# Kernel optimization log

Hardware: AMD Instinct MI355X
Metric: run time of the kernel (lower is better)

Reference implementation:

```python
import jax, jax.numpy as jnp
import numpy as np

B, S, F, DV, H, DH, L = 32, 600, 9, 1024, 16, 64, 2


def setup_inputs() -> dict:
    key = jax.random.key(0)
    ks = jax.random.split(key, 24)
    w = lambda k, shape, s=0.05: jax.random.normal(k, shape, dtype=jnp.float32) * s
    return {
        "x": w(ks[0], (B, S, F), 1.0),
        "enc_in_W": w(ks[1], (F, DV)), "enc_in_b": w(ks[2], (DV,)),
        "Wq": w(ks[3], (L, H, DV, DH)), "bq": w(ks[4], (L, H, DH)),
        "Wk": w(ks[5], (L, H, DV, DH)), "bk": w(ks[6], (L, H, DH)),
        "Wv": w(ks[7], (L, H, DV, DH)), "bv": w(ks[8], (L, H, DH)),
        "Wo": w(ks[9], (L, DV, DV)), "bo": w(ks[10], (L, DV)),
        "W1": w(ks[11], (L, DV, DV)), "b1": w(ks[12], (L, DV)),
        "W2": w(ks[13], (L, DV, DV)), "b2": w(ks[14], (L, DV)),
        "ln1_w": jnp.ones((L, DV)), "ln1_b": jnp.zeros((L, DV)),
        "ln2_w": jnp.ones((L, DV)), "ln2_b": jnp.zeros((L, DV)),
        "out_W": w(ks[15], (DV, F)), "out_b": w(ks[16], (F,)),
    }


def _layernorm(v, g, b):
    mu = v.mean(-1, keepdims=True)
    var = v.var(-1, keepdims=True)  # biased, matches torch LayerNorm
    return (v - mu) / jnp.sqrt(var + 1e-5) * g + b


def reference(x, enc_in_W, enc_in_b, Wq, bq, Wk, bk, Wv, bv, Wo, bo,
              W1, b1, W2, b2, ln1_w, ln1_b, ln2_w, ln2_b, out_W, out_b):
    # enc_input_fc; pe skipped (code checks pe_mode == 'stardard', never true)
    h = x @ enc_in_W + enc_in_b  # [B,S,DV]
    scale = 1.0 / jnp.sqrt(jnp.float32(DH))
    for l in range(L):
        q = jnp.einsum('bsd,hdk->bhsk', h, Wq[l]) + bq[l][None, :, None, :]
        k = jnp.einsum('bsd,hdk->bhsk', h, Wk[l]) + bk[l][None, :, None, :]
        v = jnp.einsum('bsd,hdk->bhsk', h, Wv[l]) + bv[l][None, :, None, :]
        attn = jax.nn.softmax(jnp.einsum('bhsk,bhtk->bhst', q, k) * scale, axis=-1)
        ctx = jnp.einsum('bhst,bhtk->bhsk', attn, v)  # [B,H,S,DH]
        # torch: stack(heads, dim=-1) -> [B,S,DH,H], then flatten(start_dim=2)
        a = ctx.transpose(0, 2, 3, 1).reshape(B, S, DH * H)
        attn_out = a @ Wo[l] + bo[l]
        x1 = _layernorm(h + attn_out, ln1_w[l], ln1_b[l])
        ff = jax.nn.elu(x1 @ W2[l] + b2[l]) @ W1[l] + b1[l]  # fc1(elu(fc2(x1)))
        h = _layernorm(x1 + ff, ln2_w[l], ln2_b[l])
    out = h @ out_W + out_b  # [B,S,F]; in_seq_len == out_seq_len -> no out_seq_fc
    return out
```

## Files before the change

kernel.cpp:

```cpp
#include <hip/hip_runtime.h>

typedef unsigned short u16;
typedef unsigned int u32;
typedef __attribute__((ext_vector_type(8))) short shortx8;
typedef __attribute__((ext_vector_type(4))) float floatx4;
typedef __attribute__((ext_vector_type(4))) u32 uintx4;
typedef __attribute__((ext_vector_type(2))) u32 uintx2;

#define AS1 __attribute__((address_space(1)))
#define AS3 __attribute__((address_space(3)))

__device__ __forceinline__ float bf2f(u16 u) {
  return __builtin_bit_cast(float, ((u32)u) << 16);
}
__device__ __forceinline__ u16 f2bf(float f) {
  u32 i = __builtin_bit_cast(u32, f);
  u32 r = (i + 0x7fffu + ((i >> 16) & 1u)) >> 16;
  return (u16)r;
}
__device__ __forceinline__ u16 f2bf_rtz(float f) {
  return (u16)(__builtin_bit_cast(u32, f) >> 16);
}

__launch_bounds__(256)
__global__ void pack_all(const float* __restrict__ Wq, const float* __restrict__ Wk,
                         const float* __restrict__ Wv, const float* __restrict__ Wo,
                         const float* __restrict__ W1, const float* __restrict__ W2,
                         const float* __restrict__ bq, const float* __restrict__ bk,
                         const float* __restrict__ bv,
                         u16* __restrict__ Bqkv, u16* __restrict__ Bwo,
                         u16* __restrict__ Bw1, u16* __restrict__ Bw2,
                         float* __restrict__ bias) {
  __shared__ u16 T[64 * 72];
  const int blk = blockIdx.x;
  const int t = threadIdx.x;

  if (blk < 1536) {
    const int which = blk >> 9, r = blk & 511;
    const int kt = r & 15, y = r >> 4;
    const float* W = (which == 0) ? Wq : (which == 1) ? Wk : Wv;
    u16* dst = Bqkv + (size_t)which * 1048576;
    const int l = y >> 4, h = y & 15;
    const int rr = t >> 2, cq = (t & 3) * 16;
    const float* src = W + ((size_t)y * 1024 + kt * 64 + rr) * 64 + cq;
#pragma unroll
    for (int e4 = 0; e4 < 4; ++e4) {
      float4 f = *(const float4*)(src + e4 * 4);
      T[(cq + e4 * 4 + 0) * 72 + rr] = f2bf(f.x);
      T[(cq + e4 * 4 + 1) * 72 + rr] = f2bf(f.y);
      T[(cq + e4 * 4 + 2) * 72 + rr] = f2bf(f.z);
      T[(cq + e4 * 4 + 3) * 72 + rr] = f2bf(f.w);
    }
    __syncthreads();
    const int dd = t >> 2, kq = (t & 3) * 16;
    u16* drow = dst + (size_t)l * 3145728 + ((size_t)h * 64 + dd) * 1024 + kt * 64 + kq;
    *(uintx4*)(drow) = *(const uintx4*)&T[dd * 72 + kq];
    *(uintx4*)(drow + 8) = *(const uintx4*)&T[dd * 72 + kq + 8];
  } else if (blk < 2048) {
    const int r = blk - 1536;
    const int l = r >> 8, rx = r & 255;
    const int rt = rx >> 4, nt = rx & 15;
    const int rr = t >> 2, cq = (t & 3) * 16;
    const float* src = Wo + (size_t)l * 1048576 + (size_t)(rt * 64 + rr) * 1024 + nt * 64 + cq;
#pragma unroll
    for (int e4 = 0; e4 < 4; ++e4) {
      float4 f = *(const float4*)(src + e4 * 4);
      T[(cq + e4 * 4 + 0) * 72 + rr] = f2bf(f.x);
      T[(cq + e4 * 4 + 1) * 72 + rr] = f2bf(f.y);
      T[(cq + e4 * 4 + 2) * 72 + rr] = f2bf(f.z);
      T[(cq + e4 * 4 + 3) * 72 + rr] = f2bf(f.w);
    }
    __syncthreads();
    const int hh = t & 15;
#pragma unroll
    for (int pass = 0; pass < 4; ++pass) {
      const int nl = pass * 16 + (t >> 4);
      uintx2 pk;
      u16 v0 = T[nl * 72 + 0 * 16 + hh], v1 = T[nl * 72 + 1 * 16 + hh];
      u16 v2 = T[nl * 72 + 2 * 16 + hh], v3 = T[nl * 72 + 3 * 16 + hh];
      pk[0] = (u32)v0 | ((u32)v1 << 16);
      pk[1] = (u32)v2 | ((u32)v3 << 16);
      *(uintx2*)&Bwo[(size_t)l * 1048576 + (size_t)(nt * 64 + nl) * 1024 + hh * 64 + rt * 4] = pk;
    }
  } else if (blk < 3072) {
    const int job = (blk - 2048) >> 9;
    const int r = (blk - 2048) & 511;
    const float* W = job == 0 ? W1 : W2;
    u16* dst = job == 0 ? Bw1 : Bw2;
    const int l = r >> 8, rx = r & 255;
    const int ct = rx & 15, rt = rx >> 4;
    const int rr = t >> 2, cq = (t & 3) * 16;
    const float* src = W + (size_t)l * 1048576 + (size_t)(rt * 64 + rr) * 1024 + ct * 64 + cq;
#pragma unroll
    for (int e4 = 0; e4 < 4; ++e4) {
      float4 f = *(const float4*)(src + e4 * 4);
      T[(cq + e4 * 4 + 0) * 72 + rr] = f2bf(f.x);
      T[(cq + e4 * 4 + 1) * 72 + rr] = f2bf(f.y);
      T[(cq + e4 * 4 + 2) * 72 + rr] = f2bf(f.z);
      T[(cq + e4 * 4 + 3) * 72 + rr] = f2bf(f.w);
    }
    __syncthreads();
    const int cc = t >> 2, rq = (t & 3) * 16;
    u16* drow = dst + (size_t)l * 1048576 + (size_t)(ct * 64 + cc) * 1024 + rt * 64 + rq;
    *(uintx4*)(drow) = *(const uintx4*)&T[cc * 72 + rq];
    *(uintx4*)(drow + 8) = *(const uintx4*)&T[cc * 72 + rq + 8];
  } else {
    const int i = (blk - 3072) * 256 + t;
    const int l = i / 3072, n = i % 3072;
    const int which = n >> 10, nn = n & 1023;
    const float* s = (which == 0) ? bq : (which == 1) ? bk : bv;
    bias[i] = s[l * 1024 + nn];
  }
}

__launch_bounds__(256)
__global__ void enc_kernel(const float* __restrict__ x, const float* __restrict__ W,
                           const float* __restrict__ bias, u16* __restrict__ h) {
  const size_t i = (size_t)blockIdx.x * 256 + threadIdx.x;
  const int m = (int)(i >> 7), nq = (int)((i & 127) << 3);
  const float* xr = x + (size_t)m * 9;
  float xv[9];
#pragma unroll
  for (int f = 0; f < 9; ++f) xv[f] = xr[f];
  u16 ov[8];
#pragma unroll
  for (int e = 0; e < 8; ++e) {
    float acc = bias[nq + e];
#pragma unroll
    for (int f = 0; f < 9; ++f) acc += xv[f] * W[f * 1024 + nq + e];
    ov[e] = f2bf(acc);
  }
  *(uintx4*)&h[(size_t)m * 1024 + nq] = *(const uintx4*)ov;
}

template <int EPI>
__launch_bounds__(512)
__global__ void gemm_bt_wide(const u16* __restrict__ A, int lda,
                             const u16* __restrict__ Bt,
                             const float* __restrict__ bias,
                             const u16* __restrict__ R, int ldr,
                             u16* __restrict__ C, int ldc) {
  constexpr int K = 1024;
  __shared__ u16 As[128 * 64];
  __shared__ u16 Bs[256 * 64];
  const int tid = threadIdx.x;
  const int lane = tid & 63;
  const int w = tid >> 6;
  const int wr = w >> 2, wc = w & 3;
  const int m0 = blockIdx.y * 128, n0 = blockIdx.x * 256;

  floatx4 acc[4][4];
#pragma unroll
  for (int i = 0; i < 4; ++i)
#pragma unroll
    for (int j = 0; j < 4; ++j) acc[i][j] = (floatx4){0.f, 0.f, 0.f, 0.f};

  const u16* Ab = A + (size_t)m0 * lda;
  const u16* Bb = Bt + (size_t)n0 * K;

  for (int k0 = 0; k0 < K; k0 += 64) {
#pragma unroll
    for (int p = 0; p < 2; ++p) {
      const int o = p * 8192 + tid * 16;
      const int row = o >> 7;
      const int ke = (o & 127) >> 1;
      __builtin_amdgcn_global_load_lds((const AS1 void*)(Ab + (size_t)row * lda + (k0 + ke)),
                                       (AS3 void*)((char*)As + o), 16, 0, 0);
    }
#pragma unroll
    for (int p = 0; p < 4; ++p) {
      const int o = p * 8192 + tid * 16;
      const int row = o >> 7;
      const int ke = (o & 127) >> 1;
      __builtin_amdgcn_global_load_lds((const AS1 void*)(Bb + (size_t)row * K + (k0 + ke)),
                                       (AS3 void*)((char*)Bs + o), 16, 0, 0);
    }
    __syncthreads();
#pragma unroll
    for (int ks = 0; ks < 2; ++ks) {
      shortx8 af[4], bfr[4];
#pragma unroll
      for (int i = 0; i < 4; ++i) {
        const int ar = wr * 64 + i * 16 + (lane & 15);
        af[i] = *(const shortx8*)&As[ar * 64 + ks * 32 + (lane >> 4) * 8];
        const int br = wc * 64 + i * 16 + (lane & 15);
        bfr[i] = *(const shortx8*)&Bs[br * 64 + ks * 32 + (lane >> 4) * 8];
      }
#pragma unroll
      for (int i = 0; i < 4; ++i)
#pragma unroll
        for (int j = 0; j < 4; ++j)
          acc[i][j] = __builtin_amdgcn_mfma_f32_16x16x32_bf16(af[i], bfr[j], acc[i][j], 0, 0, 0);
    }
    __syncthreads();
  }

  const int lr = (lane >> 4) * 4, lc = lane & 15;
#pragma unroll
  for (int i = 0; i < 4; ++i) {
#pragma unroll
    for (int j = 0; j < 4; ++j) {
      const int col = n0 + wc * 64 + j * 16 + lc;
      const float bv = bias[col];
      const bool qcol = (EPI == 3) && (col < 1024);
#pragma unroll
      for (int r = 0; r < 4; ++r) {
        const int row = m0 + wr * 64 + i * 16 + lr + r;
        float v = acc[i][j][r] + bv;
        if (EPI == 1) v += bf2f(R[(size_t)row * ldr + col]);
        if (EPI == 2) v = v > 0.f ? v : expm1f(v);
        if (EPI == 3 && qcol) v *= 0.125f;
        C[(size_t)row * ldc + col] = f2bf(v);
      }
    }
  }
}

__launch_bounds__(256)
__global__ void attn_mfma(const u16* __restrict__ qkv, u16* __restrict__ aout) {
  const int qt = blockIdx.x, bh = blockIdx.y;
  const int b = bh >> 4, h = bh & 15;
  const int tid = threadIdx.x, lane = tid & 63, w = tid >> 6;
  const int g = lane >> 4, lq = lane & 15;

  __shared__ u16 K_ld[128 * 72];
  __shared__ u16 Vt[64 * 136];
  __shared__ u16 P_ld[4][16 * 136];

  const size_t bbase = (size_t)b * 600 * 3072;
  const int q0 = qt * 128 + w * 32;

  shortx8 aq[2][2];
#pragma unroll
  for (int sub = 0; sub < 2; ++sub) {
    const int s = q0 + sub * 16 + lq;
    if (s < 600) {
      const u16* qp = qkv + bbase + (size_t)s * 3072 + h * 64 + g * 8;
      aq[sub][0] = *(const shortx8*)qp;
      aq[sub][1] = *(const shortx8*)(qp + 32);
    } else {
      aq[sub][0] = (shortx8){0, 0, 0, 0, 0, 0, 0, 0};
      aq[sub][1] = (shortx8){0, 0, 0, 0, 0, 0, 0, 0};
    }
  }

  floatx4 Oa[2][4];
  float m[2][4], l[2][4];
#pragma unroll
  for (int sub = 0; sub < 2; ++sub) {
#pragma unroll
    for (int db = 0; db < 4; ++db) Oa[sub][db] = (floatx4){0.f, 0.f, 0.f, 0.f};
#pragma unroll
    for (int r = 0; r < 4; ++r) { m[sub][r] = -1e30f; l[sub][r] = 0.f; }
  }

  for (int ch = 0; ch < 5; ++ch) {
    const int t0 = ch * 128;
    __syncthreads();
    {
      const int tloc = tid >> 1, dhalf = (tid & 1) * 32;
      const int tp = t0 + lane * 2;
      const int dq = w * 16;
      if (ch < 4) {
        const u16* kp = qkv + bbase + (size_t)(t0 + tloc) * 3072 + 1024 + h * 64 + dhalf;
#pragma unroll
        for (int c = 0; c < 4; ++c)
          *(uintx4*)&K_ld[tloc * 72 + dhalf + c * 8] = *(const uintx4*)(kp + c * 8);
        const u16* vp0 = qkv + bbase + (size_t)tp * 3072 + 2048 + h * 64 + dq;
        const u16* vp1 = vp0 + 3072;
        shortx8 r0a = *(const shortx8*)vp0;
        shortx8 r0b = *(const shortx8*)(vp0 + 8);
        shortx8 r1a = *(const shortx8*)vp1;
        shortx8 r1b = *(const shortx8*)(vp1 + 8);
#pragma unroll
        for (int e = 0; e < 8; ++e) {
          *(u32*)&Vt[(dq + e) * 136 + lane * 2] =
              (u32)(u16)r0a[e] | ((u32)(u16)r1a[e] << 16);
          *(u32*)&Vt[(dq + 8 + e) * 136 + lane * 2] =
              (u32)(u16)r0b[e] | ((u32)(u16)r1b[e] << 16);
        }
      } else {
        const int tg = t0 + tloc;
        if (tg < 600) {
          const u16* kp = qkv + bbase + (size_t)tg * 3072 + 1024 + h * 64 + dhalf;
#pragma unroll
          for (int c = 0; c < 4; ++c)
            *(uintx4*)&K_ld[tloc * 72 + dhalf + c * 8] = *(const uintx4*)(kp + c * 8);
        } else {
          const uintx4 z4 = (uintx4){0, 0, 0, 0};
#pragma unroll
          for (int c = 0; c < 4; ++c)
            *(uintx4*)&K_ld[tloc * 72 + dhalf + c * 8] = z4;
        }
        shortx8 r0a, r0b, r1a, r1b;
        if (tp < 600) {
          const u16* vp = qkv + bbase + (size_t)tp * 3072 + 2048 + h * 64 + dq;
          r0a = *(const shortx8*)vp;
          r0b = *(const shortx8*)(vp + 8);
        } else {
          r0a = (shortx8){0, 0, 0, 0, 0, 0, 0, 0};
          r0b = r0a;
        }
        if (tp + 1 < 600) {
          const u16* vp = qkv + bbase + (size_t)(tp + 1) * 3072 + 2048 + h * 64 + dq;
          r1a = *(const shortx8*)vp;
          r1b = *(const shortx8*)(vp + 8);
        } else {
          r1a = (shortx8){0, 0, 0, 0, 0, 0, 0, 0};
          r1b = r1a;
        }
#pragma unroll
        for (int e = 0; e < 8; ++e) {
          *(u32*)&Vt[(dq + e) * 136 + lane * 2] =
              (u32)(u16)r0a[e] | ((u32)(u16)r1a[e] << 16);
          *(u32*)&Vt[(dq + 8 + e) * 136 + lane * 2] =
              (u32)(u16)r0b[e] | ((u32)(u16)r1b[e] << 16);
        }
      }
    }
    __syncthreads();

#pragma unroll
    for (int sub = 0; sub < 2; ++sub) {
      floatx4 S[8];
      __builtin_amdgcn_s_setprio(1);
#pragma unroll
      for (int jb = 0; jb < 8; ++jb) {
        S[jb] = (floatx4){0.f, 0.f, 0.f, 0.f};
#pragma unroll
        for (int ks = 0; ks < 2; ++ks) {
          shortx8 bk = *(const shortx8*)&K_ld[(jb * 16 + lq) * 72 + ks * 32 + g * 8];
          S[jb] = __builtin_amdgcn_mfma_f32_16x16x32_bf16(aq[sub][ks], bk, S[jb], 0, 0, 0);
        }
      }
      __builtin_amdgcn_s_setprio(0);
      if (ch == 4) {
#pragma unroll
        for (int jb = 0; jb < 8; ++jb) {
          const bool ok = (t0 + jb * 16 + lq) < 600;
#pragma unroll
          for (int r = 0; r < 4; ++r) S[jb][r] = ok ? S[jb][r] : -1e30f;
        }
      }

      float vmax[4];
      bool need = false;
#pragma unroll
      for (int r = 0; r < 4; ++r) {
        const float v01 = fmaxf(S[0][r], S[1][r]);
        const float v23 = fmaxf(S[2][r], S[3][r]);
        const float v45 = fmaxf(S[4][r], S[5][r]);
        const float v67 = fmaxf(S[6][r], S[7][r]);
        float v = fmaxf(fmaxf(v01, v23), fmaxf(v45, v67));
        v = fmaxf(v, __shfl_xor(v, 1));
        v = fmaxf(v, __shfl_xor(v, 2));
        v = fmaxf(v, __shfl_xor(v, 4));
        v = fmaxf(v, __shfl_xor(v, 8));
        vmax[r] = v;
        need |= (v > m[sub][r] + 8.0f);
      }
      if (__any(need ? 1 : 0)) {
#pragma unroll
        for (int r = 0; r < 4; ++r) {
          const float mn = fmaxf(m[sub][r], vmax[r]);
          const float sc = __expf(m[sub][r] - mn);
          m[sub][r] = mn;
          l[sub][r] *= sc;
#pragma unroll
          for (int db = 0; db < 4; ++db) Oa[sub][db][r] *= sc;
        }
      }

      float sums[4] = {0.f, 0.f, 0.f, 0.f};
#pragma unroll
      for (int jb = 0; jb < 8; ++jb)
#pragma unroll
        for (int r = 0; r < 4; ++r) {
          const float p = __expf(S[jb][r] - m[sub][r]);
          sums[r] += p;
          P_ld[w][(g * 4 + r) * 136 + jb * 16 + lq] = f2bf_rtz(p);
        }
#pragma unroll
      for (int r = 0; r < 4; ++r) {
        float v = sums[r];
        v += __shfl_xor(v, 1);
        v += __shfl_xor(v, 2);
        v += __shfl_xor(v, 4);
        v += __shfl_xor(v, 8);
        l[sub][r] += v;
      }

      __builtin_amdgcn_s_setprio(1);
#pragma unroll
      for (int ks = 0; ks < 4; ++ks) {
        shortx8 ap = *(const shortx8*)&P_ld[w][lq * 136 + ks * 32 + g * 8];
#pragma unroll
        for (int db = 0; db < 4; ++db) {
          shortx8 bv = *(const shortx8*)&Vt[(db * 16 + lq) * 136 + ks * 32 + g * 8];
          Oa[sub][db] = __builtin_amdgcn_mfma_f32_16x16x32_bf16(ap, bv, Oa[sub][db], 0, 0, 0);
        }
      }
      __builtin_amdgcn_s_setprio(0);
    }
  }

#pragma unroll
  for (int sub = 0; sub < 2; ++sub) {
#pragma unroll
    for (int r = 0; r < 4; ++r) {
      const int sg = q0 + sub * 16 + g * 4 + r;
      if (sg < 600) {
        const float inv = 1.f / l[sub][r];
        u16* orow = aout + ((size_t)(b * 600 + sg)) * 1024 + h * 64;
#pragma unroll
        for (int db = 0; db < 4; ++db)
          orow[db * 16 + lq] = f2bf(Oa[sub][db][r] * inv);
      }
    }
  }
}

__launch_bounds__(256)
__global__ void ln_kernel(const u16* __restrict__ y, int ldy,
                          const float* __restrict__ g, const float* __restrict__ be,
                          u16* __restrict__ o, int ldo) {
  const int row = blockIdx.x, tid = threadIdx.x;
  const int lane = tid & 63, wv = tid >> 6;
  const u16* yr = y + (size_t)row * ldy;
  const int c = tid * 4;
  const uintx2 yv = *(const uintx2*)&yr[c];
  float v0 = bf2f((u16)(yv[0] & 0xffffu)), v1 = bf2f((u16)(yv[0] >> 16));
  float v2 = bf2f((u16)(yv[1] & 0xffffu)), v3 = bf2f((u16)(yv[1] >> 16));
  float s = v0 + v1 + v2 + v3;
  float q = v0 * v0 + v1 * v1 + v2 * v2 + v3 * v3;
#pragma unroll
  for (int m = 32; m; m >>= 1) {
    s += __shfl_xor(s, m);
    q += __shfl_xor(q, m);
  }
  __shared__ float red[2][4];
  if (lane == 0) {
    red[0][wv] = s;
    red[1][wv] = q;
  }
  __syncthreads();
  s = red[0][0] + red[0][1] + red[0][2] + red[0][3];
  q = red[1][0] + red[1][1] + red[1][2] + red[1][3];
  const float mu = s * (1.f / 1024.f);
  const float var = q * (1.f / 1024.f) - mu * mu;
  const float rstd = rsqrtf(var + 1e-5f);
  const float4 gv = *(const float4*)&g[c];
  const float4 bev = *(const float4*)&be[c];
  const float o0 = (v0 - mu) * rstd * gv.x + bev.x;
  const float o1 = (v1 - mu) * rstd * gv.y + bev.y;
  const float o2 = (v2 - mu) * rstd * gv.z + bev.z;
  const float o3 = (v3 - mu) * rstd * gv.w + bev.w;
  uintx2 ov;
  ov[0] = (u32)f2bf(o0) | ((u32)f2bf(o1) << 16);
  ov[1] = (u32)f2bf(o2) | ((u32)f2bf(o3) << 16);
  *(uintx2*)&o[(size_t)row * ldo + c] = ov;
}

__launch_bounds__(256)
__global__ void out_kernel(const u16* __restrict__ h, const float* __restrict__ W,
                           const float* __restrict__ bias, float* __restrict__ out) {
  const int m = blockIdx.x * 4 + (threadIdx.x >> 6);
  const int lane = threadIdx.x & 63;
  float acc[9];
#pragma unroll
  for (int f = 0; f < 9; ++f) acc[f] = 0.f;
  const u16* hr = h + (size_t)m * 1024;
#pragma unroll 4
  for (int j = 0; j < 16; ++j) {
    const int k = lane + j * 64;
    const float hv = bf2f(hr[k]);
    const float* wr = W + (size_t)k * 9;
#pragma unroll
    for (int f = 0; f < 9; ++f) acc[f] += hv * wr[f];
  }
#pragma unroll
  for (int f = 0; f < 9; ++f)
#pragma unroll
    for (int mm = 32; mm; mm >>= 1) acc[f] += __shfl_xor(acc[f], mm);
  if (lane < 9) out[(size_t)m * 9 + lane] = acc[lane] + bias[lane];
}

extern "C" void kernel_launch(void* const* d_in, const int* in_sizes, int n_in,
                              void* d_out, int out_size, void* d_ws, size_t ws_size,
                              hipStream_t stream) {
  (void)in_sizes; (void)n_in; (void)out_size; (void)ws_size;
  const float* x     = (const float*)d_in[0];
  const float* encW  = (const float*)d_in[1];
  const float* encB  = (const float*)d_in[2];
  const float* Wq    = (const float*)d_in[3];
  const float* bq    = (const float*)d_in[4];
  const float* Wk    = (const float*)d_in[5];
  const float* bk    = (const float*)d_in[6];
  const float* Wv    = (const float*)d_in[7];
  const float* bv    = (const float*)d_in[8];
  const float* Wo    = (const float*)d_in[9];
  const float* bo    = (const float*)d_in[10];
  const float* W1    = (const float*)d_in[11];
  const float* b1    = (const float*)d_in[12];
  const float* W2    = (const float*)d_in[13];
  const float* b2    = (const float*)d_in[14];
  const float* ln1w  = (const float*)d_in[15];
  const float* ln1b  = (const float*)d_in[16];
  const float* ln2w  = (const float*)d_in[17];
  const float* ln2b  = (const float*)d_in[18];
  const float* outW  = (const float*)d_in[19];
  const float* outB  = (const float*)d_in[20];
  float* out = (float*)d_out;

  char* ws = (char*)d_ws;
  size_t off = 0;
  auto alloc = [&](size_t bytes) -> void* {
    void* p = ws + off;
    off += (bytes + 255) & ~(size_t)255;
    return p;
  };
  u16* h    = (u16*)alloc(19660800ull * 2);
  u16* qkv  = (u16*)alloc(58982400ull * 2);
  u16* abuf = (u16*)alloc(19660800ull * 2);
  u16* Bqkv = (u16*)alloc(6291456ull * 2);
  u16* Bwo  = (u16*)alloc(2097152ull * 2);
  u16* Bw1  = (u16*)alloc(2097152ull * 2);
  u16* Bw2  = (u16*)alloc(2097152ull * 2);
  float* bqkv = (float*)alloc(6144ull * 4);
  u16* ybuf = qkv;
  u16* x1   = qkv + 1024;
  u16* mid  = qkv + 2048;
  u16* y2   = abuf;

  pack_all<<<3096, 256, 0, stream>>>(Wq, Wk, Wv, Wo, W1, W2, bq, bk, bv,
                                     Bqkv, Bwo, Bw1, Bw2, bqkv);
  enc_kernel<<<9600, 256, 0, stream>>>(x, encW, encB, h);

  for (int l = 0; l < 2; ++l) {
    gemm_bt_wide<3><<<dim3(12, 150), 512, 0, stream>>>(
        h, 1024, Bqkv + (size_t)l * 3145728, bqkv + l * 3072, nullptr, 0, qkv, 3072);
    attn_mfma<<<dim3(5, 512), 256, 0, stream>>>(qkv, abuf);
    gemm_bt_wide<1><<<dim3(4, 150), 512, 0, stream>>>(
        abuf, 1024, Bwo + (size_t)l * 1048576, bo + l * 1024, h, 1024, ybuf, 3072);
    ln_kernel<<<19200, 256, 0, stream>>>(ybuf, 3072, ln1w + l * 1024, ln1b + l * 1024, x1, 3072);
    gemm_bt_wide<2><<<dim3(4, 150), 512, 0, stream>>>(
        x1, 3072, Bw2 + (size_t)l * 1048576, b2 + l * 1024, nullptr, 0, mid, 3072);
    gemm_bt_wide<1><<<dim3(4, 150), 512, 0, stream>>>(
        mid, 3072, Bw1 + (size_t)l * 1048576, b1 + l * 1024, x1, 3072, y2, 1024);
    ln_kernel<<<19200, 256, 0, stream>>>(y2, 1024, ln2w + l * 1024, ln2b + l * 1024, h, 1024);
  }
  out_kernel<<<4800, 256, 0, stream>>>(h, outW, outB, out);
}
```

Measured before the change: 1.241 ms.

## Use 256x256 QKV GEMM tile and prefetch K/V chunks in attention

Adds a dedicated QKV projection kernel with a 256x256 output tile and 1024 threads per block. This halves the number of times each weight tile is reloaded across row blocks and improves operand reuse per LDS load. The attention kernel now loads the next K/V chunk into registers while the current chunk is being processed, hiding global latency behind MFMA work. The cost is higher register pressure and fewer resident blocks per CU, and the 75x12 grid gives fewer blocks to balance across CUs.

```diff
diff --git a/kernel.cpp b/kernel.cpp
--- a/kernel.cpp
+++ b/kernel.cpp
@@ -131,6 +131,85 @@
     ov[e] = f2bf(acc);
   }
   *(uintx4*)&h[(size_t)m * 1024 + nq] = *(const uintx4*)ov;
+}
+
+__launch_bounds__(1024)
+__global__ void gemm_qkv_256(const u16* __restrict__ A,
+                             const u16* __restrict__ Bt,
+                             const float* __restrict__ bias,
+                             u16* __restrict__ C) {
+  constexpr int K = 1024;
+  __shared__ u16 As[256 * 64];
+  __shared__ u16 Bs[256 * 64];
+  const int tid = threadIdx.x;
+  const int lane = tid & 63;
+  const int w = tid >> 6;
+  const int wr = w >> 2, wc = w & 3;
+  const int m0 = blockIdx.y * 256, n0 = blockIdx.x * 256;
+
+  floatx4 acc[4][4];
+#pragma unroll
+  for (int i = 0; i < 4; ++i)
+#pragma unroll
+    for (int j = 0; j < 4; ++j) acc[i][j] = (floatx4){0.f, 0.f, 0.f, 0.f};
+
+  const u16* Ab = A + (size_t)m0 * K;
+  const u16* Bb = Bt + (size_t)n0 * K;
+
+  for (int k0 = 0; k0 < K; k0 += 64) {
+#pragma unroll
+    for (int p = 0; p < 2; ++p) {
+      const int o = p * 16384 + tid * 16;
+      const int row = o >> 7;
+      const int ke = (o & 127) >> 1;
+      __builtin_amdgcn_global_load_lds((const AS1 void*)(Ab + (size_t)row * K + (k0 + ke)),
+                                       (AS3 void*)((char*)As + o), 16, 0, 0);
+    }
+#pragma unroll
+    for (int p = 0; p < 2; ++p) {
+      const int o = p * 16384 + tid * 16;
+      const int row = o >> 7;
+      const int ke = (o & 127) >> 1;
+      __builtin_amdgcn_global_load_lds((const AS1 void*)(Bb + (size_t)row * K + (k0 + ke)),
+                                       (AS3 void*)((char*)Bs + o), 16, 0, 0);
+    }
+    __syncthreads();
+#pragma unroll
+    for (int ks = 0; ks < 2; ++ks) {
+      shortx8 af[4], bfr[4];
+#pragma unroll
+      for (int i = 0; i < 4; ++i) {
+        const int ar = wr * 64 + i * 16 + (lane & 15);
+        af[i] = *(const shortx8*)&As[ar * 64 + ks * 32 + (lane >> 4) * 8];
+        const int br = wc * 64 + i * 16 + (lane & 15);
+        bfr[i] = *(const shortx8*)&Bs[br * 64 + ks * 32 + (lane >> 4) * 8];
+      }
+#pragma unroll
+      for (int i = 0; i < 4; ++i)
+#pragma unroll
+        for (int j = 0; j < 4; ++j)
+          acc[i][j] = __builtin_amdgcn_mfma_f32_16x16x32_bf16(af[i], bfr[j], acc[i][j], 0, 0, 0);
+    }
+    __syncthreads();
+  }
+
+  const int lr = (lane >> 4) * 4, lc = lane & 15;
+#pragma unroll
+  for (int i = 0; i < 4; ++i) {
+#pragma unroll
+    for (int j = 0; j < 4; ++j) {
+      const int col = n0 + wc * 64 + j * 16 + lc;
+      const float bv = bias[col];
+      const bool qcol = col < 1024;
+#pragma unroll
+      for (int r = 0; r < 4; ++r) {
+        const int row = m0 + wr * 64 + i * 16 + lr + r;
+        float v = acc[i][j][r] + bv;
+        if (qcol) v *= 0.125f;
+        C[(size_t)row * 3072 + col] = f2bf(v);
+      }
+    }
+  }
 }
 
 template <int EPI>
@@ -202,14 +281,12 @@
     for (int j = 0; j < 4; ++j) {
       const int col = n0 + wc * 64 + j * 16 + lc;
       const float bv = bias[col];
-      const bool qcol = (EPI == 3) && (col < 1024);
 #pragma unroll
       for (int r = 0; r < 4; ++r) {
         const int row = m0 + wr * 64 + i * 16 + lr + r;
         float v = acc[i][j][r] + bv;
         if (EPI == 1) v += bf2f(R[(size_t)row * ldr + col]);
         if (EPI == 2) v = v > 0.f ? v : expm1f(v);
-        if (EPI == 3 && qcol) v *= 0.125f;
         C[(size_t)row * ldc + col] = f2bf(v);
       }
     }
@@ -229,6 +306,8 @@
 
   const size_t bbase = (size_t)b * 600 * 3072;
   const int q0 = qt * 128 + w * 32;
+  const int tloc = tid >> 1, dhalf = (tid & 1) * 32;
+  const int dq = w * 16;
 
   shortx8 aq[2][2];
 #pragma unroll
@@ -254,70 +333,68 @@
     for (int r = 0; r < 4; ++r) { m[sub][r] = -1e30f; l[sub][r] = 0.f; }
   }
 
+  uintx4 kreg[4];
+  shortx8 vra, vrb, vrc, vrd;
+
+  auto LOADC = [&](int ch) {
+    const int t0 = ch * 128;
+    if (ch < 4) {
+      const u16* kp = qkv + bbase + (size_t)(t0 + tloc) * 3072 + 1024 + h * 64 + dhalf;
+#pragma unroll
+      for (int c = 0; c < 4; ++c) kreg[c] = *(const uintx4*)(kp + c * 8);
+      const u16* vp0 = qkv + bbase + (size_t)(t0 + lane * 2) * 3072 + 2048 + h * 64 + dq;
+      vra = *(const shortx8*)vp0;
+      vrb = *(const shortx8*)(vp0 + 8);
+      vrc = *(const shortx8*)(vp0 + 3072);
+      vrd = *(const shortx8*)(vp0 + 3072 + 8);
+    } else {
+      const int tg = t0 + tloc;
+      if (tg < 600) {
+        const u16* kp = qkv + bbase + (size_t)tg * 3072 + 1024 + h * 64 + dhalf;
+#pragma unroll
+        for (int c = 0; c < 4; ++c) kreg[c] = *(const uintx4*)(kp + c * 8);
+      } else {
+#pragma unroll
+        for (int c = 0; c < 4; ++c) kreg[c] = (uintx4){0, 0, 0, 0};
+      }
+      const int tp = t0 + lane * 2;
+      if (tp < 600) {
+        const u16* vp = qkv + bbase + (size_t)tp * 3072 + 2048 + h * 64 + dq;
+        vra = *(const shortx8*)vp;
+        vrb = *(const shortx8*)(vp + 8);
+      } else {
+        vra = (shortx8){0, 0, 0, 0, 0, 0, 0, 0};
+        vrb = vra;
+      }
+      if (tp + 1 < 600) {
+        const u16* vp = qkv + bbase + (size_t)(tp + 1) * 3072 + 2048 + h * 64 + dq;
+        vrc = *(const shortx8*)vp;
+        vrd = *(const shortx8*)(vp + 8);
+      } else {
+        vrc = (shortx8){0, 0, 0, 0, 0, 0, 0, 0};
+        vrd = vrc;
+      }
+    }
+  };
+  auto WRITEC = [&]() {
+#pragma unroll
+    for (int c = 0; c < 4; ++c)
+      *(uintx4*)&K_ld[tloc * 72 + dhalf + c * 8] = kreg[c];
+#pragma unroll
+    for (int e = 0; e < 8; ++e) {
+      *(u32*)&Vt[(dq + e) * 136 + lane * 2] =
+          (u32)(u16)vra[e] | ((u32)(u16)vrc[e] << 16);
+      *(u32*)&Vt[(dq + 8 + e) * 136 + lane * 2] =
+          (u32)(u16)vrb[e] | ((u32)(u16)vrd[e] << 16);
+    }
+  };
+
+  LOADC(0);
   for (int ch = 0; ch < 5; ++ch) {
     const int t0 = ch * 128;
     __syncthreads();
-    {
-      const int tloc = tid >> 1, dhalf = (tid & 1) * 32;
-      const int tp = t0 + lane * 2;
-      const int dq = w * 16;
-      if (ch < 4) {
-        const u16* kp = qkv + bbase + (size_t)(t0 + tloc) * 3072 + 1024 + h * 64 + dhalf;
-#pragma unroll
-        for (int c = 0; c < 4; ++c)
-          *(uintx4*)&K_ld[tloc * 72 + dhalf + c * 8] = *(const uintx4*)(kp + c * 8);
-        const u16* vp0 = qkv + bbase + (size_t)tp * 3072 + 2048 + h * 64 + dq;
-        const u16* vp1 = vp0 + 3072;
-        shortx8 r0a = *(const shortx8*)vp0;
-        shortx8 r0b = *(const shortx8*)(vp0 + 8);
-        shortx8 r1a = *(const shortx8*)vp1;
-        shortx8 r1b = *(const shortx8*)(vp1 + 8);
-#pragma unroll
-        for (int e = 0; e < 8; ++e) {
-          *(u32*)&Vt[(dq + e) * 136 + lane * 2] =
-              (u32)(u16)r0a[e] | ((u32)(u16)r1a[e] << 16);
-          *(u32*)&Vt[(dq + 8 + e) * 136 + lane * 2] =
-              (u32)(u16)r0b[e] | ((u32)(u16)r1b[e] << 16);
-        }
-      } else {
-        const int tg = t0 + tloc;
-        if (tg < 600) {
-          const u16* kp = qkv + bbase + (size_t)tg * 3072 + 1024 + h * 64 + dhalf;
-#pragma unroll
-          for (int c = 0; c < 4; ++c)
-            *(uintx4*)&K_ld[tloc * 72 + dhalf + c * 8] = *(const uintx4*)(kp + c * 8);
-        } else {
-          const uintx4 z4 = (uintx4){0, 0, 0, 0};
-#pragma unroll
-          for (int c = 0; c < 4; ++c)
-            *(uintx4*)&K_ld[tloc * 72 + dhalf + c * 8] = z4;
-        }
-        shortx8 r0a, r0b, r1a, r1b;
-        if (tp < 600) {
-          const u16* vp = qkv + bbase + (size_t)tp * 3072 + 2048 + h * 64 + dq;
-          r0a = *(const shortx8*)vp;
-          r0b = *(const shortx8*)(vp + 8);
-        } else {
-          r0a = (shortx8){0, 0, 0, 0, 0, 0, 0, 0};
-          r0b = r0a;
-        }
-        if (tp + 1 < 600) {
-          const u16* vp = qkv + bbase + (size_t)(tp + 1) * 3072 + 2048 + h * 64 + dq;
-          r1a = *(const shortx8*)vp;
-          r1b = *(const shortx8*)(vp + 8);
-        } else {
-          r1a = (shortx8){0, 0, 0, 0, 0, 0, 0, 0};
-          r1b = r1a;
-        }
-#pragma unroll
-        for (int e = 0; e < 8; ++e) {
-          *(u32*)&Vt[(dq + e) * 136 + lane * 2] =
-              (u32)(u16)r0a[e] | ((u32)(u16)r1a[e] << 16);
-          *(u32*)&Vt[(dq + 8 + e) * 136 + lane * 2] =
-              (u32)(u16)r0b[e] | ((u32)(u16)r1b[e] << 16);
-        }
-      }
-    }
+    WRITEC();
+    if (ch < 4) LOADC(ch + 1);
     __syncthreads();
 
 #pragma unroll
@@ -537,8 +614,8 @@
   enc_kernel<<<9600, 256, 0, stream>>>(x, encW, encB, h);
 
   for (int l = 0; l < 2; ++l) {
-    gemm_bt_wide<3><<<dim3(12, 150), 512, 0, stream>>>(
-        h, 1024, Bqkv + (size_t)l * 3145728, bqkv + l * 3072, nullptr, 0, qkv, 3072);
+    gemm_qkv_256<<<dim3(12, 75), 1024, 0, stream>>>(
+        h, Bqkv + (size_t)l * 3145728, bqkv + l * 3072, qkv);
     attn_mfma<<<dim3(5, 512), 256, 0, stream>>>(qkv, abuf);
     gemm_bt_wide<1><<<dim3(4, 150), 512, 0, stream>>>(
         abuf, 1024, Bwo + (size_t)l * 1048576, bo + l * 1024, h, 1024, ybuf, 3072);
```

Result: slower. 1.328 ms (+7.0%).
